# Optimization experiments

Measured on AMD Instinct MI355X. Metric: run time of the kernel, lower is better.

Reference implementation:

```python
import jax, jax.numpy as jnp
import numpy as np

B, V, C, M, CM, D, OUT = 16, 16, 64, 32, 16, 128, 600
VOCAB = {"cond": 4000, "proc": 2000, "drug": 600, "lab_item": 700, "lab_value": 2000, "inj_item": 400, "inj_value": 2000}


def _gru(x, Wih, Whh, bih, bhh):
    """Batch-first torch-style GRU. x: [N,T,D] -> (outputs [N,T,D], h_T [N,D])."""
    Dh = Whh.shape[1]

    def step(h, xt):
        gi = xt @ Wih.T + bih
        gh = h @ Whh.T + bhh
        ir, iz, ig = jnp.split(gi, 3, axis=-1)
        hr, hz, hg = jnp.split(gh, 3, axis=-1)
        r = jax.nn.sigmoid(ir + hr)
        z = jax.nn.sigmoid(iz + hz)
        n = jnp.tanh(ig + r * hg)
        h = (1.0 - z) * n + z * h
        return h, h

    h0 = jnp.zeros((x.shape[0], Dh), x.dtype)
    hT, ys = jax.lax.scan(step, h0, jnp.swapaxes(x, 0, 1))
    return jnp.swapaxes(ys, 0, 1), hT


def _hetero_mp(feats, Wself, Wmsg):
    """Heterogeneous message passing over node types on the fully-connected
    monitor<->visit-feature bipartite pattern: each node type combines a self
    transform with a transformed mean of the other node types, then ReLU.
    feats: list of [N,D]; Wself/Wmsg: [T,D,D]."""
    stacked = jnp.stack(feats)  # [T,N,D]
    total = jnp.sum(stacked, axis=0)
    T = stacked.shape[0]
    outs = []
    for t in range(T):
        others = (total - stacked[t]) / (T - 1)
        outs.append(jax.nn.relu(stacked[t] @ Wself[t] + others @ Wmsg[t]))
    return outs


def _forward(codes_cond, codes_proc, codes_drug, codes_lab_item, codes_lab_value,
             codes_inj_item, codes_inj_value, weight, age,
             emb_cond, emb_proc, emb_drug, emb_lab_item, emb_lab_value,
             emb_inj_item, emb_inj_value,
             mgru_Wih, mgru_Whh, mgru_bih, mgru_bhh,
             vgru_Wih, vgru_Whh, vgru_bih, vgru_bhh,
             gnn_Wself, gnn_Wmsg,
             fc_weight_W, fc_weight_b, fc_age_W, fc_age_b,
             fc_patient_W, fc_patient_b):
    # ---- visit-event features: embedding lookup + sum-pool over codes ----
    vis = {}
    for k, codes, emb in (("cond", codes_cond, emb_cond),
                          ("proc", codes_proc, emb_proc),
                          ("drug", codes_drug, emb_drug)):
        vis[k] = jnp.sum(emb[codes], axis=2)  # [B,V,D]
    visit_keys = ("cond", "proc", "drug")

    # ---- monitor-event pairs: (item * value) embeddings, GNN, two-level GRU ----
    pairs = (
        (codes_lab_item, codes_lab_value, emb_lab_item, emb_lab_value, "lab_item", (0, 2, 3, 4)),
        (codes_inj_item, codes_inj_value, emb_inj_item, emb_inj_value, "inj_item", (1, 2, 3, 4)),
    )
    hid = {}
    for p, (ci, cv, ei, ev, ikey, gidx) in enumerate(pairs):
        mon = jnp.sum(ei[ci] * ev[cv], axis=3)  # [B,V,M,D]
        feats = [mon.reshape(-1, D)]  # monitor node type, [B*V*M, D]
        for k in visit_keys:  # visit features repeated across monitors
            feats.append(jnp.broadcast_to(vis[k][:, :, None, :], (B, V, M, D)).reshape(-1, D))
        outs = _hetero_mp(feats, gnn_Wself[p], gnn_Wmsg[p])
        for t, k in enumerate((ikey,) + visit_keys):
            g = gidx[t]
            # monitor-level GRU over the M monitors of each visit
            o, _ = _gru(outs[t].reshape(B * V, M, D), mgru_Wih[g], mgru_Whh[g], mgru_bih[g], mgru_bhh[g])
            last = o[:, -1, :].reshape(B, V, D)  # last monitor state per visit
            # visit-level GRU (source uses visit_gru[feature_key1] for all keys)
            _, h = _gru(last, vgru_Wih[p], vgru_Whh[p], vgru_bih[p], vgru_bhh[p])
            hid[k] = h if k not in hid else hid[k] + h

    # ---- weight / age scalar features ----
    for k, x, W, b, vi in (("weight", weight, fc_weight_W, fc_weight_b, 2),
                           ("age", age, fc_age_W, fc_age_b, 3)):
        mask = (x != 0.0)[..., None]  # [B,V,1]
        xe = (x[..., None] * W[:, 0] + b) * mask  # Linear(1->D) then zero-mask
        _, h = _gru(xe, vgru_Wih[vi], vgru_Whh[vi], vgru_bih[vi], vgru_bhh[vi])
        hid[k] = h

    # ---- concat in dict-insertion order, then ReLU + Linear head ----
    pe = jnp.concatenate([hid["lab_item"], hid["cond"], hid["proc"], hid["drug"],
                          hid["inj_item"], hid["weight"], hid["age"]], axis=-1)  # [B, 7D]
    return jax.nn.relu(pe) @ fc_patient_W.T + fc_patient_b  # [B, OUT]


def setup_inputs() -> dict:
    key = jax.random.key(0)
    ks = iter(jax.random.split(key, 64))

    def nrm(shape, s=0.1):
        return (jax.random.normal(next(ks), shape) * s).astype(jnp.float32)

    def emb_table(vsz):
        t = nrm((vsz, D), 1.0)
        return t.at[0].set(0.0)  # padding_idx=0 row is zero

    inp = {}
    inp["codes_cond"] = jax.random.randint(next(ks), (B, V, C), 0, VOCAB["cond"], dtype=jnp.int32)
    inp["codes_proc"] = jax.random.randint(next(ks), (B, V, C), 0, VOCAB["proc"], dtype=jnp.int32)
    inp["codes_drug"] = jax.random.randint(next(ks), (B, V, C), 0, VOCAB["drug"], dtype=jnp.int32)
    inp["codes_lab_item"] = jax.random.randint(next(ks), (B, V, M, CM), 0, VOCAB["lab_item"], dtype=jnp.int32)
    inp["codes_lab_value"] = jax.random.randint(next(ks), (B, V, M, CM), 0, VOCAB["lab_value"], dtype=jnp.int32)
    inp["codes_inj_item"] = jax.random.randint(next(ks), (B, V, M, CM), 0, VOCAB["inj_item"], dtype=jnp.int32)
    inp["codes_inj_value"] = jax.random.randint(next(ks), (B, V, M, CM), 0, VOCAB["inj_value"], dtype=jnp.int32)
    inp["weight"] = jax.random.uniform(next(ks), (B, V), minval=0.1, maxval=1.0, dtype=jnp.float32)
    inp["age"] = jax.random.uniform(next(ks), (B, V), minval=0.1, maxval=1.0, dtype=jnp.float32)
    inp["emb_cond"] = emb_table(VOCAB["cond"])
    inp["emb_proc"] = emb_table(VOCAB["proc"])
    inp["emb_drug"] = emb_table(VOCAB["drug"])
    inp["emb_lab_item"] = emb_table(VOCAB["lab_item"])
    inp["emb_lab_value"] = emb_table(VOCAB["lab_value"])
    inp["emb_inj_item"] = emb_table(VOCAB["inj_item"])
    inp["emb_inj_value"] = emb_table(VOCAB["inj_value"])
    inp["mgru_Wih"] = nrm((5, 3 * D, D))
    inp["mgru_Whh"] = nrm((5, 3 * D, D))
    inp["mgru_bih"] = nrm((5, 3 * D))
    inp["mgru_bhh"] = nrm((5, 3 * D))
    inp["vgru_Wih"] = nrm((4, 3 * D, D))
    inp["vgru_Whh"] = nrm((4, 3 * D, D))
    inp["vgru_bih"] = nrm((4, 3 * D))
    inp["vgru_bhh"] = nrm((4, 3 * D))
    inp["gnn_Wself"] = nrm((2, 4, D, D))
    inp["gnn_Wmsg"] = nrm((2, 4, D, D))
    inp["fc_weight_W"] = nrm((D, 1))
    inp["fc_weight_b"] = nrm((D,))
    inp["fc_age_W"] = nrm((D, 1))
    inp["fc_age_b"] = nrm((D,))
    inp["fc_patient_W"] = nrm((OUT, 7 * D))
    inp["fc_patient_b"] = nrm((OUT,))
    return inp


def reference(codes_cond, codes_proc, codes_drug, codes_lab_item, codes_lab_value,
              codes_inj_item, codes_inj_value, weight, age,
              emb_cond, emb_proc, emb_drug, emb_lab_item, emb_lab_value,
              emb_inj_item, emb_inj_value,
              mgru_Wih, mgru_Whh, mgru_bih, mgru_bhh,
              vgru_Wih, vgru_Whh, vgru_bih, vgru_bhh,
              gnn_Wself, gnn_Wmsg,
              fc_weight_W, fc_weight_b, fc_age_W, fc_age_b,
              fc_patient_W, fc_patient_b):
    return _forward(codes_cond, codes_proc, codes_drug, codes_lab_item, codes_lab_value,
                    codes_inj_item, codes_inj_value, weight, age,
                    emb_cond, emb_proc, emb_drug, emb_lab_item, emb_lab_value,
                    emb_inj_item, emb_inj_value,
                    mgru_Wih, mgru_Whh, mgru_bih, mgru_bhh,
                    vgru_Wih, vgru_Whh, vgru_bih, vgru_bhh,
                    gnn_Wself, gnn_Wmsg,
                    fc_weight_W, fc_weight_b, fc_age_W, fc_age_b,
                    fc_patient_W, fc_patient_b)
```

## Files before the change

kernel.cpp:

```cpp
#include <hip/hip_runtime.h>
#include <math.h>

#define B_   16
#define V_   16
#define C_   64
#define M_   32
#define CM_  16
#define D_   128
#define OUT_ 600
#define NSEQ 256
#define NROW 8192

typedef __attribute__((ext_vector_type(8))) short bf16x8;
typedef __attribute__((ext_vector_type(4))) short bf16x4;
typedef __attribute__((ext_vector_type(4))) float f32x4;

__device__ __forceinline__ unsigned short f2bf(float x) {
  union { float f; unsigned u; } v; v.f = x;
  unsigned r = v.u + 0x7fff + ((v.u >> 16) & 1);
  return (unsigned short)(r >> 16);
}
__device__ __forceinline__ float bf2f(short s) {
  union { unsigned u; float f; } v;
  v.u = ((unsigned)(unsigned short)s) << 16;
  return v.f;
}
__device__ __forceinline__ float fsig(float x)  { return __fdividef(1.f, 1.f + __expf(-x)); }
__device__ __forceinline__ float ftanh(float x) { return 1.f - 2.f*__fdividef(1.f, __expf(2.f*x) + 1.f); }

__device__ __forceinline__ void ldsbar() {
  asm volatile("s_waitcnt lgkmcnt(0)" ::: "memory");
  __builtin_amdgcn_s_barrier();
  asm volatile("" ::: "memory");
}

constexpr int OFF_VISB  = 98304;
constexpr int OFF_MONB  = 147456;
constexpr int OFF_W12T  = 2244608;
constexpr int OFF_WIHB  = 2375680;
constexpr int OFF_WIHTV = 2498560;
constexpr int OFF_XE    = 2695168;
constexpr int OFF_LAST  = 27926528;
constexpr int OFF_VH    = 29171712;

__global__ __launch_bounds__(256) void k_prepvis(
    const float* __restrict__ Wself, const float* __restrict__ Wmsg,
    const float* __restrict__ mWih,  const float* __restrict__ vWih,
    const float* __restrict__ wgt,   const float* __restrict__ age,
    const float* __restrict__ fwW,   const float* __restrict__ fwB,
    const float* __restrict__ faW,   const float* __restrict__ faB,
    const int* __restrict__ cc, const int* __restrict__ cp, const int* __restrict__ cd,
    const float* __restrict__ ec, const float* __restrict__ ep, const float* __restrict__ ed,
    const int* __restrict__ cli, const int* __restrict__ clv,
    const int* __restrict__ cii, const int* __restrict__ civ,
    const float* __restrict__ eli, const float* __restrict__ elv,
    const float* __restrict__ eii, const float* __restrict__ eiv,
    short* __restrict__ w12t, short* __restrict__ wihb,
    float* __restrict__ wihTv, float* __restrict__ xe,
    short* __restrict__ visb, short* __restrict__ monb)
{
  int bx = blockIdx.x, tid = threadIdx.x;
  if (bx < 1024) {
    int lin = bx*256 + tid;
    int pt = lin >> 15, rem = lin & 32767;
    int n = rem >> 8, k = rem & 255;
    float v;
    if (k < 128) v = Wself[pt*16384 + k*128 + n] - Wmsg[pt*16384 + k*128 + n]*(1.f/3.f);
    else         v = Wmsg[pt*16384 + (k-128)*128 + n]*(1.f/3.f);
    w12t[lin] = (short)f2bf(v);
  } else if (bx < 1984) {
    int lin = (bx-1024)*256 + tid;
    wihb[lin] = (short)f2bf(mWih[lin]);
  } else if (bx < 2752) {
    int lin = (bx-1984)*256 + tid;
    int g = lin / 49152, rem2 = lin % 49152;
    int k = rem2 / 384, j = rem2 % 384;
    wihTv[lin] = vWih[g*49152 + j*128 + k];
  } else if (bx < 3008) {
    int lin = (bx-2752)*256 + tid;
    int which = lin >> 15, rem2 = lin & 32767;
    int n = rem2 >> 7, d = rem2 & 127;
    float x  = which ? age[n] : wgt[n];
    float Wv = which ? faW[d] : fwW[d];
    float bb = which ? faB[d] : fwB[d];
    xe[lin] = (x != 0.0f) ? (x*Wv + bb) : 0.0f;
  } else if (bx < 3392) {
    int idx = (bx-3008)*256 + tid;
    int type = idx >> 15;
    int r = idx & 32767;
    int bv = r >> 7, d = r & 127;
    const int*   codes = (type==0) ? cc : (type==1) ? cp : cd;
    const float* emb   = (type==0) ? ec : (type==1) ? ep : ed;
    float acc = 0.f;
    for (int c = 0; c < C_; ++c) {
      int code = codes[bv*C_ + c];
      acc += emb[code*D_ + d];
    }
    visb[(type*NSEQ + bv)*D_ + d] = (short)f2bf(acc);
  } else {
    int rowid = (bx-3392)*2 + (tid >> 7);
    int p = rowid >> 13, bvm = rowid & 8191;
    int d = tid & 127;
    const int* ci = p ? cii : cli;  const int* cv = p ? civ : clv;
    const float* ei = p ? eii : eli; const float* ev = p ? eiv : elv;
    float acc = 0.f;
    #pragma unroll
    for (int c2 = 0; c2 < CM_; ++c2) {
      int iv = ci[bvm*CM_ + c2];
      int vv = cv[bvm*CM_ + c2];
      acc += ei[iv*D_ + d] * ev[vv*D_ + d];
    }
    monb[((size_t)p*NROW + bvm)*D_ + d] = (short)f2bf(acc);
  }
}

__global__ __launch_bounds__(512, 1) void k_ggru(
    const short* __restrict__ monb, const short* __restrict__ visb,
    const short* __restrict__ w12t, const short* __restrict__ wihb,
    const float* __restrict__ Wself, const float* __restrict__ mWhh,
    const float* __restrict__ mbih, const float* __restrict__ mbhh,
    float* __restrict__ last)
{
  const int run  = blockIdx.x >> 4;
  const int pair = blockIdx.x & 15;
  const int p = run >> 2, t = run & 3;
  const int g = (run % 4 == 0) ? (run / 4) : (run % 4 + 1);
  const int tid = threadIdx.x;
  const int w = tid >> 6;
  const int lane = tid & 63;
  const int c = lane & 15, q = lane >> 4;
  const int j = w*16 + c;

  __shared__ short hb[2][4][16][40];
  __shared__ __align__(16) short Ys[2][16][136];
  __shared__ __align__(16) short Xl[2][2048];

  for (int idx = tid; idx < 2*4*16*40; idx += 512)
    ((short*)hb)[idx] = 0;

  bf16x8 bW12[8];
  #pragma unroll
  for (int kt = 0; kt < 8; ++kt)
    bW12[kt] = *(const bf16x8*)(w12t + (size_t)run*32768 + (size_t)j*256 + kt*32 + q*8);

  bf16x8 bWs[4];
  if (t == 0) {
    const float* wsp = Wself + (size_t)run*16384 + j;
    #pragma unroll
    for (int kt = 0; kt < 4; ++kt) {
      bf16x8 tt;
      #pragma unroll
      for (int i = 0; i < 8; ++i)
        tt[i] = (short)f2bf(wsp[(kt*32 + q*8 + i)*128]);
      bWs[kt] = tt;
    }
  } else {
    #pragma unroll
    for (int kt = 0; kt < 4; ++kt) bWs[kt] = bW12[kt+4];
  }

  f32x4 Cpre = (f32x4){0.f,0.f,0.f,0.f};
  {
    const int bvc = pair*16 + c;
    #pragma unroll
    for (int kt = 0; kt < 4; ++kt) {
      const int ko = kt*32 + q*8;
      bf16x8 v0 = *(const bf16x8*)(visb + (size_t)(0*NSEQ + bvc)*128 + ko);
      bf16x8 v1 = *(const bf16x8*)(visb + (size_t)(1*NSEQ + bvc)*128 + ko);
      bf16x8 v2 = *(const bf16x8*)(visb + (size_t)(2*NSEQ + bvc)*128 + ko);
      bf16x8 vs;
      #pragma unroll
      for (int i = 0; i < 8; ++i)
        vs[i] = (short)f2bf(bf2f(v0[i]) + bf2f(v1[i]) + bf2f(v2[i]));
      Cpre = __builtin_amdgcn_mfma_f32_16x16x32_bf16(vs, bW12[kt+4], Cpre, 0, 0, 0);
    }
    if (t > 0) {
      #pragma unroll
      for (int kt = 0; kt < 4; ++kt) {
        const int ko = kt*32 + q*8;
        bf16x8 fv = *(const bf16x8*)(visb + (size_t)((t-1)*NSEQ + bvc)*128 + ko);
        Cpre = __builtin_amdgcn_mfma_f32_16x16x32_bf16(fv, bW12[kt], Cpre, 0, 0, 0);
      }
    }
  }

  bf16x8 bWih[3][4];
  #pragma unroll
  for (int gate = 0; gate < 3; ++gate)
    #pragma unroll
    for (int kt = 0; kt < 4; ++kt)
      bWih[gate][kt] = *(const bf16x8*)(wihb + ((size_t)g*384 + gate*128 + j)*128 + kt*32 + q*8);

  bf16x8 bWhh[3][4];
  #pragma unroll
  for (int gate = 0; gate < 3; ++gate) {
    const float* wp = mWhh + ((size_t)g*384 + gate*128 + j)*128 + q*8;
    #pragma unroll
    for (int kt = 0; kt < 4; ++kt) {
      float4 lo = *(const float4*)(wp + kt*32);
      float4 hi = *(const float4*)(wp + kt*32 + 4);
      bf16x8 tt;
      tt[0]=(short)f2bf(lo.x); tt[1]=(short)f2bf(lo.y); tt[2]=(short)f2bf(lo.z); tt[3]=(short)f2bf(lo.w);
      tt[4]=(short)f2bf(hi.x); tt[5]=(short)f2bf(hi.y); tt[6]=(short)f2bf(hi.z); tt[7]=(short)f2bf(hi.w);
      bWhh[gate][kt] = tt;
    }
  }
  const float bs0 = mbih[g*384 +       j] + mbhh[g*384 +       j];
  const float bs1 = mbih[g*384 + 128 + j] + mbhh[g*384 + 128 + j];
  const float bi2 = mbih[g*384 + 256 + j];
  const float bh2 = mbhh[g*384 + 256 + j];

  const bool stg = (tid < 256);
  const int xr_ = (tid >> 4) & 15, xu = tid & 15;
  const int bv = pair*16 + xr_;
  const short* fsrc = monb + ((size_t)p*NROW + (size_t)bv*32)*128 + xu*8;
  const int xdofs = xr_*128 + (((xu*16) ^ ((xr_&7)<<4)) >> 1);
  short* xdst0 = &Xl[0][xdofs];
  short* xdst1 = &Xl[1][xdofs];

  if (stg) {
    *(bf16x8*)xdst0 = *(const bf16x8*)fsrc;
    *(bf16x8*)xdst1 = *(const bf16x8*)(fsrc + 128);
  }
  float hf[4] = {0.f,0.f,0.f,0.f};
  const int ktw = w >> 1;
  const int kkw = (w & 1)*16 + c;
  ldsbar();

  {
    const char* xbase = (const char*)&Xl[0][0];
    f32x4 accY = Cpre;
    #pragma unroll
    for (int kt = 0; kt < 4; ++kt) {
      bf16x8 aX = *(const bf16x8*)(xbase + c*256 + ((kt*64 + q*16) ^ ((c&7)<<4)));
      accY = __builtin_amdgcn_mfma_f32_16x16x32_bf16(aX, bWs[kt], accY, 0, 0, 0);
    }
    #pragma unroll
    for (int reg = 0; reg < 4; ++reg)
      Ys[0][q*4 + reg][w*16 + c] = (short)f2bf(fmaxf(accY[reg], 0.f));
  }
  ldsbar();

  #pragma unroll 1
  for (int m = 0; m < 32; ++m) {
    const int cur = m & 1, nxt = cur ^ 1;

    bf16x8 xnext;
    if (stg && m < 30) xnext = *(const bf16x8*)(fsrc + (size_t)(m+2)*128);

    f32x4 accY = Cpre;
    if (m < 31) {
      const char* xbase = (const char*)&Xl[nxt][0];
      #pragma unroll
      for (int kt = 0; kt < 4; ++kt) {
        bf16x8 aX = *(const bf16x8*)(xbase + c*256 + ((kt*64 + q*16) ^ ((c&7)<<4)));
        accY = __builtin_amdgcn_mfma_f32_16x16x32_bf16(aX, bWs[kt], accY, 0, 0, 0);
      }
    }

    bf16x8 ah[4], a2[4];
    #pragma unroll
    for (int kt = 0; kt < 4; ++kt) {
      ah[kt] = *(const bf16x8*)&hb[cur][kt][c][q*8];
      a2[kt] = *(const bf16x8*)&Ys[cur][c][kt*32 + q*8];
    }
    f32x4 acc0 = (f32x4){0.f,0.f,0.f,0.f};
    f32x4 acc1 = (f32x4){0.f,0.f,0.f,0.f};
    f32x4 aG2  = (f32x4){0.f,0.f,0.f,0.f};
    f32x4 aH2  = (f32x4){0.f,0.f,0.f,0.f};
    #pragma unroll
    for (int kt = 0; kt < 4; ++kt) {
      acc0 = __builtin_amdgcn_mfma_f32_16x16x32_bf16(ah[kt], bWhh[0][kt], acc0, 0, 0, 0);
      acc1 = __builtin_amdgcn_mfma_f32_16x16x32_bf16(ah[kt], bWhh[1][kt], acc1, 0, 0, 0);
      aH2  = __builtin_amdgcn_mfma_f32_16x16x32_bf16(ah[kt], bWhh[2][kt], aH2,  0, 0, 0);
    }
    #pragma unroll
    for (int kt = 0; kt < 4; ++kt) {
      acc0 = __builtin_amdgcn_mfma_f32_16x16x32_bf16(a2[kt], bWih[0][kt], acc0, 0, 0, 0);
      acc1 = __builtin_amdgcn_mfma_f32_16x16x32_bf16(a2[kt], bWih[1][kt], acc1, 0, 0, 0);
      aG2  = __builtin_amdgcn_mfma_f32_16x16x32_bf16(a2[kt], bWih[2][kt], aG2,  0, 0, 0);
    }

    if (m < 31) {
      #pragma unroll
      for (int reg = 0; reg < 4; ++reg)
        Ys[nxt][q*4 + reg][w*16 + c] = (short)f2bf(fmaxf(accY[reg], 0.f));
    }
    if (stg && m < 30) *(bf16x8*)(cur ? xdst1 : xdst0) = xnext;

    #pragma unroll
    for (int reg = 0; reg < 4; ++reg) {
      float rr = fsig(acc0[reg] + bs0);
      float zz = fsig(acc1[reg] + bs1);
      float nn = ftanh(aG2[reg] + bi2 + rr*(aH2[reg] + bh2));
      float hnew = (1.f - zz)*nn + zz*hf[reg];
      hf[reg] = hnew;
      hb[nxt][ktw][q*4 + reg][kkw] = (short)f2bf(hnew);
    }
    ldsbar();
  }

  #pragma unroll
  for (int reg = 0; reg < 4; ++reg)
    last[((size_t)run*NSEQ + pair*16 + q*4 + reg)*D_ + j] = hf[reg];
}

__global__ __launch_bounds__(768) void k_vgru(
    const float* __restrict__ last, const float* __restrict__ xe,
    const float* __restrict__ wihTv, const float* __restrict__ vbih,
    const float* __restrict__ vWhh, const float* __restrict__ vbhh,
    float* __restrict__ vh)
{
  int run = blockIdx.x >> 4, b = blockIdx.x & 15;
  int tid = threadIdx.x;
  int vidx = (run < 4) ? 0 : (run < 8) ? 1 : (run - 6);

  __shared__ float Xs[16][128];
  __shared__ float giL[16*384];
  __shared__ __align__(16) float hsv[128];
  __shared__ float gh[384];

  const float* X = (run < 8) ? (last + ((size_t)run*NSEQ + b*16)*D_)
                             : (xe + ((size_t)(run-8)*NSEQ + b*16)*D_);
  for (int idx = tid; idx < 2048; idx += 768)
    ((float*)Xs)[idx] = X[idx];
  if (tid < 128) hsv[tid] = 0.f;
  __syncthreads();

  {
    int half = (tid >= 384) ? 1 : 0;
    int j = tid - half*384;
    float accv[8];
    float bias = vbih[vidx*384 + j];
    #pragma unroll
    for (int s = 0; s < 8; ++s) accv[s] = bias;
    const float* W = wihTv + vidx*49152 + j;
    #pragma unroll 4
    for (int k = 0; k < 128; ++k) {
      float wv = W[k*384];
      #pragma unroll
      for (int s = 0; s < 8; ++s) accv[s] += Xs[half*8 + s][k] * wv;
    }
    #pragma unroll
    for (int s = 0; s < 8; ++s)
      giL[(half*8 + s)*384 + j] = accv[s];
  }

  int j = tid >> 1, kh = tid & 1;
  float w[64];
  const float4* wrow = (const float4*)(vWhh + (vidx*384 + j)*128 + kh*64);
  #pragma unroll
  for (int k4 = 0; k4 < 16; ++k4) {
    float4 t4 = wrow[k4];
    w[4*k4] = t4.x; w[4*k4+1] = t4.y; w[4*k4+2] = t4.z; w[4*k4+3] = t4.w;
  }
  float bj = vbhh[vidx*384 + j];
  __syncthreads();

  #pragma unroll 1
  for (int v = 0; v < 16; ++v) {
    const float4* h4 = (const float4*)(hsv + kh*64);
    float p0 = 0.f, p1 = 0.f;
    #pragma unroll
    for (int k4 = 0; k4 < 8; ++k4) {
      float4 u0 = h4[k4], u1 = h4[k4+8];
      p0 += w[4*k4   ]*u0.x + w[4*k4+1 ]*u0.y + w[4*k4+2 ]*u0.z + w[4*k4+3 ]*u0.w;
      p1 += w[4*k4+32]*u1.x + w[4*k4+33]*u1.y + w[4*k4+34]*u1.z + w[4*k4+35]*u1.w;
    }
    float part = p0 + p1;
    part += __shfl_xor(part, 1);
    if (kh == 0) gh[j] = bj + ((j < 256) ? giL[v*384 + j] : 0.f) + part;
    __syncthreads();
    if (tid < 128) {
      float r = fsig(gh[tid]);
      float z = fsig(gh[tid+128]);
      float gin = giL[v*384 + 256 + tid];
      float n = ftanh(gin + r*gh[tid+256]);
      hsv[tid] = (1.f - z)*n + z*hsv[tid];
    }
    __syncthreads();
  }
  if (tid < 128) vh[(run*16 + b)*D_ + tid] = hsv[tid];
}

__global__ __launch_bounds__(256) void k_head(
    const float* __restrict__ vh, const float* __restrict__ Wp,
    const float* __restrict__ bp, float* __restrict__ out)
{
  const int o = blockIdx.x;
  const int tid = threadIdx.x;
  const int b = tid & 15, kc = tid >> 4;
  const int a1[7] = {0,1,2,3,4,8,9};
  const int a2[7] = {-1,5,6,7,-1,-1,-1};
  const float4* wb = (const float4*)(Wp + (size_t)o*896 + kc*56);
  float acc = 0.f;
  #pragma unroll
  for (int i = 0; i < 14; ++i) {
    int cc2 = kc*56 + i*4;
    int s = cc2 >> 7, d0 = cc2 & 127;
    float4 a = *(const float4*)(vh + (a1[s]*16 + b)*D_ + d0);
    int s2 = a2[s];
    if (s2 >= 0) {
      float4 a2v = *(const float4*)(vh + (s2*16 + b)*D_ + d0);
      a.x += a2v.x; a.y += a2v.y; a.z += a2v.z; a.w += a2v.w;
    }
    a.x = fmaxf(a.x, 0.f); a.y = fmaxf(a.y, 0.f);
    a.z = fmaxf(a.z, 0.f); a.w = fmaxf(a.w, 0.f);
    float4 ww = wb[i];
    acc += a.x*ww.x + a.y*ww.y + a.z*ww.z + a.w*ww.w;
  }
  __shared__ float red[16][17];
  red[kc][b] = acc;
  __syncthreads();
  if (tid < 16) {
    float s = 0.f;
    #pragma unroll
    for (int k = 0; k < 16; ++k) s += red[k][tid];
    out[tid*OUT_ + o] = s + bp[o];
  }
}

extern "C" void kernel_launch(void* const* d_in, const int* in_sizes, int n_in,
                              void* d_out, int out_size, void* d_ws, size_t ws_size,
                              hipStream_t stream)
{
  (void)in_sizes; (void)n_in; (void)out_size; (void)ws_size;
  const int*   cc   = (const int*)  d_in[0];
  const int*   cp   = (const int*)  d_in[1];
  const int*   cd   = (const int*)  d_in[2];
  const int*   cli  = (const int*)  d_in[3];
  const int*   clv  = (const int*)  d_in[4];
  const int*   cii  = (const int*)  d_in[5];
  const int*   civ  = (const int*)  d_in[6];
  const float* wgt  = (const float*)d_in[7];
  const float* age  = (const float*)d_in[8];
  const float* ec   = (const float*)d_in[9];
  const float* ep   = (const float*)d_in[10];
  const float* ed   = (const float*)d_in[11];
  const float* eli  = (const float*)d_in[12];
  const float* elv  = (const float*)d_in[13];
  const float* eii  = (const float*)d_in[14];
  const float* eiv  = (const float*)d_in[15];
  const float* mWih = (const float*)d_in[16];
  const float* mWhh = (const float*)d_in[17];
  const float* mbih = (const float*)d_in[18];
  const float* mbhh = (const float*)d_in[19];
  const float* vWih = (const float*)d_in[20];
  const float* vWhh = (const float*)d_in[21];
  const float* vbih = (const float*)d_in[22];
  const float* vbhh = (const float*)d_in[23];
  const float* Wself= (const float*)d_in[24];
  const float* Wmsg = (const float*)d_in[25];
  const float* fwW  = (const float*)d_in[26];
  const float* fwB  = (const float*)d_in[27];
  const float* faW  = (const float*)d_in[28];
  const float* faB  = (const float*)d_in[29];
  const float* Wp   = (const float*)d_in[30];
  const float* bp   = (const float*)d_in[31];
  float* out = (float*)d_out;
  float* ws  = (float*)d_ws;

  short* visb  = (short*)(ws + OFF_VISB);
  short* monb  = (short*)(ws + OFF_MONB);
  short* w12t  = (short*)(ws + OFF_W12T);
  short* wihb  = (short*)(ws + OFF_WIHB);
  float* wihTv = ws + OFF_WIHTV;
  float* xe    = ws + OFF_XE;
  float* last  = ws + OFF_LAST;
  float* vh    = ws + OFF_VH;

  k_prepvis<<<11584, 256, 0, stream>>>(Wself, Wmsg, mWih, vWih, wgt, age,
                                       fwW, fwB, faW, faB,
                                       cc, cp, cd, ec, ep, ed,
                                       cli, clv, cii, civ, eli, elv, eii, eiv,
                                       w12t, wihb, wihTv, xe, visb, monb);
  k_ggru<<<128, 512, 0, stream>>>(monb, visb, w12t, wihb, Wself,
                                  mWhh, mbih, mbhh, last);
  k_vgru<<<160, 768, 0, stream>>>(last, xe, wihTv, vbih, vWhh, vbhh, vh);
  k_head<<<600, 256, 0, stream>>>(vh, Wp, bp, out);
}
```

Baseline: 244.8 us.

## Rewrite visit GRU with bf16 MFMA, batching 16 sequences per block

The visit-level GRU kernel changes from one block per (run, batch) sequence using fp32 scalar dot products to one block per run that handles all 16 batch sequences at once. Both the input and recurrent projections now use bf16 16x16x32 MFMA with weights held in registers. The per-step input projection is software-pipelined one step ahead, with X double-buffered in swizzled LDS. This removes the large fp32 precompute and the 768-thread scalar recurrence, but cuts the grid from 160 to 10 blocks and adds bf16 rounding error.

```diff
diff --git a/kernel.cpp b/kernel.cpp
--- a/kernel.cpp
+++ b/kernel.cpp
@@ -305,82 +305,138 @@
     last[((size_t)run*NSEQ + pair*16 + q*4 + reg)*D_ + j] = hf[reg];
 }
 
-__global__ __launch_bounds__(768) void k_vgru(
+__global__ __launch_bounds__(512, 1) void k_vgru(
     const float* __restrict__ last, const float* __restrict__ xe,
-    const float* __restrict__ wihTv, const float* __restrict__ vbih,
-    const float* __restrict__ vWhh, const float* __restrict__ vbhh,
+    const float* __restrict__ vWih, const float* __restrict__ vWhh,
+    const float* __restrict__ vbih, const float* __restrict__ vbhh,
     float* __restrict__ vh)
 {
-  int run = blockIdx.x >> 4, b = blockIdx.x & 15;
-  int tid = threadIdx.x;
-  int vidx = (run < 4) ? 0 : (run < 8) ? 1 : (run - 6);
-
-  __shared__ float Xs[16][128];
-  __shared__ float giL[16*384];
-  __shared__ __align__(16) float hsv[128];
-  __shared__ float gh[384];
-
-  const float* X = (run < 8) ? (last + ((size_t)run*NSEQ + b*16)*D_)
-                             : (xe + ((size_t)(run-8)*NSEQ + b*16)*D_);
-  for (int idx = tid; idx < 2048; idx += 768)
-    ((float*)Xs)[idx] = X[idx];
-  if (tid < 128) hsv[tid] = 0.f;
-  __syncthreads();
-
+  const int run = blockIdx.x;
+  const int vidx = (run < 4) ? 0 : (run < 8) ? 1 : (run - 6);
+  const int tid = threadIdx.x;
+  const int w = tid >> 6;
+  const int lane = tid & 63;
+  const int c = lane & 15, q = lane >> 4;
+  const int j = w*16 + c;
+
+  __shared__ short hb[2][4][16][40];
+  __shared__ __align__(16) short Xl[2][2048];
+
+  for (int idx = tid; idx < 2*4*16*40; idx += 512)
+    ((short*)hb)[idx] = 0;
+
+  bf16x8 bWih[3][4], bWhh[3][4];
+  #pragma unroll
+  for (int gate = 0; gate < 3; ++gate) {
+    const float* wi = vWih + ((size_t)vidx*384 + gate*128 + j)*128 + q*8;
+    const float* wh = vWhh + ((size_t)vidx*384 + gate*128 + j)*128 + q*8;
+    #pragma unroll
+    for (int kt = 0; kt < 4; ++kt) {
+      float4 a0 = *(const float4*)(wi + kt*32);
+      float4 a1 = *(const float4*)(wi + kt*32 + 4);
+      float4 b0 = *(const float4*)(wh + kt*32);
+      float4 b1 = *(const float4*)(wh + kt*32 + 4);
+      bf16x8 ti, th;
+      ti[0]=(short)f2bf(a0.x); ti[1]=(short)f2bf(a0.y); ti[2]=(short)f2bf(a0.z); ti[3]=(short)f2bf(a0.w);
+      ti[4]=(short)f2bf(a1.x); ti[5]=(short)f2bf(a1.y); ti[6]=(short)f2bf(a1.z); ti[7]=(short)f2bf(a1.w);
+      th[0]=(short)f2bf(b0.x); th[1]=(short)f2bf(b0.y); th[2]=(short)f2bf(b0.z); th[3]=(short)f2bf(b0.w);
+      th[4]=(short)f2bf(b1.x); th[5]=(short)f2bf(b1.y); th[6]=(short)f2bf(b1.z); th[7]=(short)f2bf(b1.w);
+      bWih[gate][kt] = ti;
+      bWhh[gate][kt] = th;
+    }
+  }
+  const float bs0 = vbih[vidx*384 +       j] + vbhh[vidx*384 +       j];
+  const float bs1 = vbih[vidx*384 + 128 + j] + vbhh[vidx*384 + 128 + j];
+  const float bi2 = vbih[vidx*384 + 256 + j];
+  const float bh2 = vbhh[vidx*384 + 256 + j];
+
+  const bool stg = (tid < 256);
+  const int xr_ = (tid >> 4) & 15, xu = tid & 15;
+  const float* xsrc = ((run < 8) ? (last + ((size_t)run*NSEQ + xr_*16)*D_)
+                                 : (xe + ((size_t)(run-8)*NSEQ + xr_*16)*D_)) + xu*8;
+  const int xdofs = xr_*128 + (((xu*16) ^ ((xr_&7)<<4)) >> 1);
+  short* xdst0 = &Xl[0][xdofs];
+  short* xdst1 = &Xl[1][xdofs];
+
+  auto stageX = [&](short* dst, int v) {
+    const float* s = xsrc + (size_t)v*D_;
+    float4 lo = *(const float4*)s;
+    float4 hi = *(const float4*)(s + 4);
+    bf16x8 t;
+    t[0]=(short)f2bf(lo.x); t[1]=(short)f2bf(lo.y); t[2]=(short)f2bf(lo.z); t[3]=(short)f2bf(lo.w);
+    t[4]=(short)f2bf(hi.x); t[5]=(short)f2bf(hi.y); t[6]=(short)f2bf(hi.z); t[7]=(short)f2bf(hi.w);
+    *(bf16x8*)dst = t;
+  };
+  if (stg) { stageX(xdst0, 0); stageX(xdst1, 1); }
+
+  float hf[4] = {0.f,0.f,0.f,0.f};
+  const int ktw = w >> 1;
+  const int kkw = (w & 1)*16 + c;
+  ldsbar();
+
+  f32x4 giA[3], giB[3];
   {
-    int half = (tid >= 384) ? 1 : 0;
-    int j = tid - half*384;
-    float accv[8];
-    float bias = vbih[vidx*384 + j];
-    #pragma unroll
-    for (int s = 0; s < 8; ++s) accv[s] = bias;
-    const float* W = wihTv + vidx*49152 + j;
-    #pragma unroll 4
-    for (int k = 0; k < 128; ++k) {
-      float wv = W[k*384];
-      #pragma unroll
-      for (int s = 0; s < 8; ++s) accv[s] += Xs[half*8 + s][k] * wv;
-    }
-    #pragma unroll
-    for (int s = 0; s < 8; ++s)
-      giL[(half*8 + s)*384 + j] = accv[s];
-  }
-
-  int j = tid >> 1, kh = tid & 1;
-  float w[64];
-  const float4* wrow = (const float4*)(vWhh + (vidx*384 + j)*128 + kh*64);
-  #pragma unroll
-  for (int k4 = 0; k4 < 16; ++k4) {
-    float4 t4 = wrow[k4];
-    w[4*k4] = t4.x; w[4*k4+1] = t4.y; w[4*k4+2] = t4.z; w[4*k4+3] = t4.w;
-  }
-  float bj = vbhh[vidx*384 + j];
-  __syncthreads();
+    const char* xbase = (const char*)&Xl[0][0];
+    #pragma unroll
+    for (int gate = 0; gate < 3; ++gate) giA[gate] = (f32x4){0.f,0.f,0.f,0.f};
+    #pragma unroll
+    for (int kt = 0; kt < 4; ++kt) {
+      bf16x8 ax = *(const bf16x8*)(xbase + c*256 + ((kt*64 + q*16) ^ ((c&7)<<4)));
+      giA[0] = __builtin_amdgcn_mfma_f32_16x16x32_bf16(ax, bWih[0][kt], giA[0], 0, 0, 0);
+      giA[1] = __builtin_amdgcn_mfma_f32_16x16x32_bf16(ax, bWih[1][kt], giA[1], 0, 0, 0);
+      giA[2] = __builtin_amdgcn_mfma_f32_16x16x32_bf16(ax, bWih[2][kt], giA[2], 0, 0, 0);
+    }
+  }
+  ldsbar();
+
+  auto step = [&](int v, f32x4 (&gcur)[3], f32x4 (&gnext)[3]) {
+    const int cur = v & 1, nxt = cur ^ 1;
+    if (v < 15) {
+      const char* xbase = (const char*)&Xl[nxt][0];
+      #pragma unroll
+      for (int gate = 0; gate < 3; ++gate) gnext[gate] = (f32x4){0.f,0.f,0.f,0.f};
+      #pragma unroll
+      for (int kt = 0; kt < 4; ++kt) {
+        bf16x8 ax = *(const bf16x8*)(xbase + c*256 + ((kt*64 + q*16) ^ ((c&7)<<4)));
+        gnext[0] = __builtin_amdgcn_mfma_f32_16x16x32_bf16(ax, bWih[0][kt], gnext[0], 0, 0, 0);
+        gnext[1] = __builtin_amdgcn_mfma_f32_16x16x32_bf16(ax, bWih[1][kt], gnext[1], 0, 0, 0);
+        gnext[2] = __builtin_amdgcn_mfma_f32_16x16x32_bf16(ax, bWih[2][kt], gnext[2], 0, 0, 0);
+      }
+    }
+    bf16x8 ah[4];
+    #pragma unroll
+    for (int kt = 0; kt < 4; ++kt)
+      ah[kt] = *(const bf16x8*)&hb[cur][kt][c][q*8];
+    f32x4 a0 = gcur[0], a1 = gcur[1];
+    f32x4 aH2 = (f32x4){0.f,0.f,0.f,0.f};
+    #pragma unroll
+    for (int kt = 0; kt < 4; ++kt) {
+      a0  = __builtin_amdgcn_mfma_f32_16x16x32_bf16(ah[kt], bWhh[0][kt], a0,  0, 0, 0);
+      a1  = __builtin_amdgcn_mfma_f32_16x16x32_bf16(ah[kt], bWhh[1][kt], a1,  0, 0, 0);
+      aH2 = __builtin_amdgcn_mfma_f32_16x16x32_bf16(ah[kt], bWhh[2][kt], aH2, 0, 0, 0);
+    }
+    if (stg && v < 14) stageX(cur ? xdst1 : xdst0, v + 2);
+    #pragma unroll
+    for (int reg = 0; reg < 4; ++reg) {
+      float rr = fsig(a0[reg] + bs0);
+      float zz = fsig(a1[reg] + bs1);
+      float nn = ftanh(gcur[2][reg] + bi2 + rr*(aH2[reg] + bh2));
+      float hnew = (1.f - zz)*nn + zz*hf[reg];
+      hf[reg] = hnew;
+      hb[nxt][ktw][q*4 + reg][kkw] = (short)f2bf(hnew);
+    }
+    ldsbar();
+  };
 
   #pragma unroll 1
-  for (int v = 0; v < 16; ++v) {
-    const float4* h4 = (const float4*)(hsv + kh*64);
-    float p0 = 0.f, p1 = 0.f;
-    #pragma unroll
-    for (int k4 = 0; k4 < 8; ++k4) {
-      float4 u0 = h4[k4], u1 = h4[k4+8];
-      p0 += w[4*k4   ]*u0.x + w[4*k4+1 ]*u0.y + w[4*k4+2 ]*u0.z + w[4*k4+3 ]*u0.w;
-      p1 += w[4*k4+32]*u1.x + w[4*k4+33]*u1.y + w[4*k4+34]*u1.z + w[4*k4+35]*u1.w;
-    }
-    float part = p0 + p1;
-    part += __shfl_xor(part, 1);
-    if (kh == 0) gh[j] = bj + ((j < 256) ? giL[v*384 + j] : 0.f) + part;
-    __syncthreads();
-    if (tid < 128) {
-      float r = fsig(gh[tid]);
-      float z = fsig(gh[tid+128]);
-      float gin = giL[v*384 + 256 + tid];
-      float n = ftanh(gin + r*gh[tid+256]);
-      hsv[tid] = (1.f - z)*n + z*hsv[tid];
-    }
-    __syncthreads();
-  }
-  if (tid < 128) vh[(run*16 + b)*D_ + tid] = hsv[tid];
+  for (int v2 = 0; v2 < 8; ++v2) {
+    step(2*v2,     giA, giB);
+    step(2*v2 + 1, giB, giA);
+  }
+
+  #pragma unroll
+  for (int reg = 0; reg < 4; ++reg)
+    vh[((size_t)run*16 + q*4 + reg)*D_ + j] = hf[reg];
 }
 
 __global__ __launch_bounds__(256) void k_head(
@@ -476,6 +532,6 @@
                                        w12t, wihb, wihTv, xe, visb, monb);
   k_ggru<<<128, 512, 0, stream>>>(monb, visb, w12t, wihb, Wself,
                                   mWhh, mbih, mbhh, last);
-  k_vgru<<<160, 768, 0, stream>>>(last, xe, wihTv, vbih, vWhh, vbhh, vh);
+  k_vgru<<<10, 512, 0, stream>>>(last, xe, vWih, vWhh, vbih, vbhh, vh);
   k_head<<<600, 256, 0, stream>>>(vh, Wp, bp, out);
 }
```

Measured after the change: 245.9 us. No clear change (+0.5%).
